# Kernel tuning notes

Measured on AMD Instinct MI355X. Metric: run time of the kernel, lower is better.

## Reference

```python
import jax, jax.numpy as jnp
import numpy as np

B, N, E, H = 2, 4096, 512, 8
D = E // H  # head size


def setup_inputs() -> dict:
    key = jax.random.key(0)
    ks = jax.random.split(key, 11)
    s = 1.0 / np.sqrt(E)
    inp = {
        'q': jax.random.normal(ks[0], (B, N, E), jnp.float32),
        'k': jax.random.normal(ks[1], (B, N, E), jnp.float32),
        'v': jax.random.normal(ks[2], (B, N, E), jnp.float32),
        'Wq': jax.random.uniform(ks[3], (E, E), jnp.float32, -s, s),
        'bq': jax.random.uniform(ks[4], (E,), jnp.float32, -s, s),
        'Wk': jax.random.uniform(ks[5], (E, E), jnp.float32, -s, s),
        'bk': jax.random.uniform(ks[6], (E,), jnp.float32, -s, s),
        'Wv': jax.random.uniform(ks[7], (E, E), jnp.float32, -s, s),
        'bv': jax.random.uniform(ks[8], (E,), jnp.float32, -s, s),
        'Wo': jax.random.uniform(ks[9], (E, E), jnp.float32, -s, s),
        'bo': jax.random.uniform(ks[10], (E,), jnp.float32, -s, s),
    }
    return inp


def reference(q, k, v, Wq, bq, Wk, bk, Wv, bv, Wo, bo):
    # Linear projections (torch Linear: x @ W.T + b)
    qp = (q @ Wq.T + bq).reshape(B, N, H, D).transpose(0, 2, 1, 3)  # [B,H,N,D]
    kp = (k @ Wk.T + bk).reshape(B, N, H, D).transpose(0, 2, 1, 3)
    vp = (v @ Wv.T + bv).reshape(B, N, H, D).transpose(0, 2, 1, 3)
    scores = jnp.einsum('bhnd,bhmd->bhnm', qp, kp) / jnp.sqrt(jnp.float32(D))
    attn = jax.nn.softmax(scores, axis=-1)
    out = jnp.einsum('bhnm,bhmd->bhnd', attn, vp)  # [B,H,N,D]
    out = out.transpose(0, 2, 1, 3).reshape(B, N, E)
    return out @ Wo.T + bo
```

## Files before the change

kernel.cpp:

```cpp
#include <hip/hip_runtime.h>
#include <hip/hip_bf16.h>
#include <cstddef>
#include <cstdint>


typedef __bf16 bf16_t;
typedef __bf16 bf16x8 __attribute__((ext_vector_type(8)));
typedef __bf16 bf16x4 __attribute__((ext_vector_type(4)));
typedef float  f32x4  __attribute__((ext_vector_type(4)));

#define MFMA_BF16 __builtin_amdgcn_mfma_f32_16x16x32_bf16

static __device__ __forceinline__ bf16x8 cvt2(const float4& a, const float4& b) {
  return bf16x8{(bf16_t)a.x,(bf16_t)a.y,(bf16_t)a.z,(bf16_t)a.w,
                (bf16_t)b.x,(bf16_t)b.y,(bf16_t)b.z,(bf16_t)b.w};
}

static __device__ __forceinline__ uint32_t pk2(float a, float b) {
  uint32_t r;
  asm("v_cvt_pk_bf16_f32 %0, %1, %2" : "=v"(r) : "v"(a), "v"(b));
  return r;
}

__global__ void __launch_bounds__(256)
cvt_bf16(const float* __restrict__ q, const float* __restrict__ k,
         const float* __restrict__ v, const float* __restrict__ Wq,
         const float* __restrict__ Wk, const float* __restrict__ Wv,
         const float* __restrict__ Wo,
         bf16_t* __restrict__ qb, bf16_t* __restrict__ kb,
         bf16_t* __restrict__ vb, bf16_t* __restrict__ wq,
         bf16_t* __restrict__ wk, bf16_t* __restrict__ wv,
         bf16_t* __restrict__ wo)
{
  const int CQ = 524288;
  const int CW = 32768;
  const int TOT = 3 * CQ + 4 * CW;
  const int STRIDE = 2048 * 256;
  for (int c = blockIdx.x * 256 + threadIdx.x; c < TOT; c += STRIDE) {
    const float* src; bf16_t* dst; int off;
    if (c < 3 * CQ) {
      const int t = c >> 19;
      const int r = c & (CQ - 1);
      src = (t == 0) ? q : (t == 1) ? k : v;
      dst = (t == 0) ? qb : (t == 1) ? kb : vb;
      off = r << 3;
    } else {
      const int c2 = c - 3 * CQ;
      const int t = c2 >> 15;
      const int r = c2 & (CW - 1);
      src = (t == 0) ? Wq : (t == 1) ? Wk : (t == 2) ? Wv : Wo;
      dst = (t == 0) ? wq : (t == 1) ? wk : (t == 2) ? wv : wo;
      off = r << 3;
    }
    const float4 a = *(const float4*)(src + off);
    const float4 b = *(const float4*)(src + off + 4);
    *(bf16x8*)(dst + off) = cvt2(a, b);
  }
}

__global__ void __launch_bounds__(256, 3)
qkv_proj(const bf16_t* __restrict__ qb, const bf16_t* __restrict__ kb,
         const bf16_t* __restrict__ vb,
         const bf16_t* __restrict__ Wqb, const float* __restrict__ bq,
         const bf16_t* __restrict__ Wkb, const float* __restrict__ bk,
         const bf16_t* __restrict__ Wvb, const float* __restrict__ bv,
         bf16_t* __restrict__ Qp, bf16_t* __restrict__ Kp,
         bf16_t* __restrict__ Vt, float qscale)
{
  __shared__ __align__(16) bf16_t S[2 * 128 * 72];
  bf16_t* As = S;
  bf16_t* Bs = S + 128 * 72;

  const int l     = blockIdx.x;
  const int slice = l >> 8;
  const int inner = l & 255;
  const int mtile = ((inner >> 5) << 3) | (inner & 7);
  const int ntile = (inner >> 3) & 3;
  const int tid   = threadIdx.x;
  const int w     = tid >> 6;
  const int lane  = tid & 63;
  const int lr    = lane & 15;
  const int quad  = lane >> 4;
  const int wm    = w & 1;
  const int wn    = w >> 1;
  const int xrow  = tid >> 1, xcol = (tid & 1) << 5;

  const bf16_t* Xb   = (slice == 0) ? qb  : (slice == 1) ? kb  : vb;
  const bf16_t* W    = (slice == 0) ? Wqb : (slice == 1) ? Wkb : Wvb;
  const float*  bias = (slice == 0) ? bq  : (slice == 1) ? bk  : bv;
  const float scale  = (slice == 0) ? qscale : 1.0f;

  float bvv[4];
#pragma unroll
  for (int ci = 0; ci < 4; ++ci) bvv[ci] = bias[ntile * 128 + wn * 64 + ci * 16 + lr];

  f32x4 acc[4][4] = {};
  bf16x8 xa[4], wa[4];

#pragma unroll
  for (int j = 0; j < 4; ++j) {
    xa[j] = *(const bf16x8*)(Xb + (size_t)(mtile * 128 + xrow) * 512 + xcol + j * 8);
    wa[j] = *(const bf16x8*)(W  + (size_t)(ntile * 128 + xrow) * 512 + xcol + j * 8);
  }
#pragma unroll
  for (int j = 0; j < 4; ++j) {
    *(bf16x8*)(&As[xrow * 72 + xcol + j * 8]) = xa[j];
    *(bf16x8*)(&Bs[xrow * 72 + xcol + j * 8]) = wa[j];
  }
  __syncthreads();

  for (int it = 0; it < 8; ++it) {
    if (it != 7) {
      const int k0 = (it + 1) << 6;
#pragma unroll
      for (int j = 0; j < 4; ++j) {
        xa[j] = *(const bf16x8*)(Xb + (size_t)(mtile * 128 + xrow) * 512 + k0 + xcol + j * 8);
        wa[j] = *(const bf16x8*)(W  + (size_t)(ntile * 128 + xrow) * 512 + k0 + xcol + j * 8);
      }
    }
    bf16x8 af[4][2], bfr[4][2];
#pragma unroll
    for (int mi = 0; mi < 4; ++mi)
#pragma unroll
      for (int kh = 0; kh < 2; ++kh)
        af[mi][kh] = *(const bf16x8*)(&As[(wm * 64 + mi * 16 + lr) * 72 + (kh * 4 + quad) * 8]);
#pragma unroll
    for (int ci = 0; ci < 4; ++ci)
#pragma unroll
      for (int kh = 0; kh < 2; ++kh)
        bfr[ci][kh] = *(const bf16x8*)(&Bs[(wn * 64 + ci * 16 + lr) * 72 + (kh * 4 + quad) * 8]);
#pragma unroll
    for (int mi = 0; mi < 4; ++mi)
#pragma unroll
      for (int ci = 0; ci < 4; ++ci) {
        acc[mi][ci] = MFMA_BF16(af[mi][0], bfr[ci][0], acc[mi][ci], 0, 0, 0);
        acc[mi][ci] = MFMA_BF16(af[mi][1], bfr[ci][1], acc[mi][ci], 0, 0, 0);
      }
    __syncthreads();
    if (it != 7) {
#pragma unroll
      for (int j = 0; j < 4; ++j) {
        *(bf16x8*)(&As[xrow * 72 + xcol + j * 8]) = xa[j];
        *(bf16x8*)(&Bs[xrow * 72 + xcol + j * 8]) = wa[j];
      }
      __syncthreads();
    }
  }

  bf16_t (*Ct)[136] = (bf16_t (*)[136])S;
  if (slice < 2) {
    bf16_t* outQK = (slice == 0) ? Qp : Kp;
#pragma unroll
    for (int mi = 0; mi < 4; ++mi)
#pragma unroll
      for (int ci = 0; ci < 4; ++ci)
#pragma unroll
        for (int r = 0; r < 4; ++r)
          Ct[wm * 64 + mi * 16 + quad * 4 + r][wn * 64 + ci * 16 + lr] =
              (bf16_t)((acc[mi][ci][r] + bvv[ci]) * scale);
    __syncthreads();
    const int r2 = tid >> 1, half = tid & 1;
    const int gm = mtile * 128 + r2;
    const int b = gm >> 12, n = gm & 4095;
    const int gc0 = ntile * 128 + half * 64;
    const int h = gc0 >> 6;
    bf16_t* dst = outQK + (size_t)((b * 8 + h) * 4096 + n) * 64;
#pragma unroll
    for (int j = 0; j < 8; ++j)
      *(bf16x8*)(dst + j * 8) = *(const bf16x8*)(&Ct[r2][half * 64 + j * 8]);
  } else {
#pragma unroll
    for (int mi = 0; mi < 4; ++mi)
#pragma unroll
      for (int ci = 0; ci < 4; ++ci)
#pragma unroll
        for (int r = 0; r < 4; ++r)
          Ct[wn * 64 + ci * 16 + lr][wm * 64 + mi * 16 + quad * 4 + r] =
              (bf16_t)(acc[mi][ci][r] + bvv[ci]);
    __syncthreads();
    const int dline = tid >> 1, half = tid & 1;
    const int gc = ntile * 128 + dline;
    const int h = gc >> 6, dd = gc & 63;
    const int b = (mtile * 128) >> 12;
    const int n0 = (mtile * 128) & 4095;
    bf16_t* dst = Vt + (size_t)((b * 8 + h) * 64 + dd) * 4096 + n0 + half * 64;
#pragma unroll
    for (int j = 0; j < 8; ++j)
      *(bf16x8*)(dst + j * 8) = *(const bf16x8*)(&Ct[dline][half * 64 + j * 8]);
  }
}

__global__ void __launch_bounds__(256, 4)
o_proj(const bf16_t* __restrict__ Xb, const bf16_t* __restrict__ W,
       const float* __restrict__ bias, float* __restrict__ out)
{
  __shared__ __align__(16) bf16_t As[64 * 72];
  __shared__ __align__(16) bf16_t Bs[64 * 72];
  const int l     = blockIdx.x;
  const int mtile = l >> 3;
  const int ntile = l & 7;
  const int tid   = threadIdx.x;
  const int w     = tid >> 6;
  const int lane  = tid & 63;
  const int lr    = lane & 15;
  const int quad  = lane >> 4;
  const int wm    = w & 1;
  const int wn    = w >> 1;
  const int xrow  = tid >> 2, xcol = (tid & 3) << 4;

  float bvv[2];
#pragma unroll
  for (int ci = 0; ci < 2; ++ci) bvv[ci] = bias[ntile * 64 + wn * 32 + ci * 16 + lr];

  f32x4 acc[2][2] = {};
  bf16x8 xb[2], wb[2];

#pragma unroll
  for (int j = 0; j < 2; ++j) {
    xb[j] = *(const bf16x8*)(Xb + (size_t)(mtile * 64 + xrow) * 512 + xcol + j * 8);
    wb[j] = *(const bf16x8*)(W  + (size_t)(ntile * 64 + xrow) * 512 + xcol + j * 8);
  }
#pragma unroll
  for (int j = 0; j < 2; ++j) {
    *(bf16x8*)(&As[xrow * 72 + xcol + j * 8]) = xb[j];
    *(bf16x8*)(&Bs[xrow * 72 + xcol + j * 8]) = wb[j];
  }
  __syncthreads();

  for (int it = 0; it < 8; ++it) {
    if (it != 7) {
      const int k0 = (it + 1) << 6;
#pragma unroll
      for (int j = 0; j < 2; ++j) {
        xb[j] = *(const bf16x8*)(Xb + (size_t)(mtile * 64 + xrow) * 512 + k0 + xcol + j * 8);
        wb[j] = *(const bf16x8*)(W  + (size_t)(ntile * 64 + xrow) * 512 + k0 + xcol + j * 8);
      }
    }
    bf16x8 af[2][2], bfr[2][2];
#pragma unroll
    for (int mi = 0; mi < 2; ++mi)
#pragma unroll
      for (int kh = 0; kh < 2; ++kh)
        af[mi][kh] = *(const bf16x8*)(&As[(wm * 32 + mi * 16 + lr) * 72 + (kh * 4 + quad) * 8]);
#pragma unroll
    for (int ci = 0; ci < 2; ++ci)
#pragma unroll
      for (int kh = 0; kh < 2; ++kh)
        bfr[ci][kh] = *(const bf16x8*)(&Bs[(wn * 32 + ci * 16 + lr) * 72 + (kh * 4 + quad) * 8]);
#pragma unroll
    for (int mi = 0; mi < 2; ++mi)
#pragma unroll
      for (int ci = 0; ci < 2; ++ci) {
        acc[mi][ci] = MFMA_BF16(af[mi][0], bfr[ci][0], acc[mi][ci], 0, 0, 0);
        acc[mi][ci] = MFMA_BF16(af[mi][1], bfr[ci][1], acc[mi][ci], 0, 0, 0);
      }
    __syncthreads();
    if (it != 7) {
#pragma unroll
      for (int j = 0; j < 2; ++j) {
        *(bf16x8*)(&As[xrow * 72 + xcol + j * 8]) = xb[j];
        *(bf16x8*)(&Bs[xrow * 72 + xcol + j * 8]) = wb[j];
      }
      __syncthreads();
    }
  }

#pragma unroll
  for (int mi = 0; mi < 2; ++mi) {
    const int gm0 = mtile * 64 + wm * 32 + mi * 16 + quad * 4;
#pragma unroll
    for (int ci = 0; ci < 2; ++ci) {
      const int gc = ntile * 64 + wn * 32 + ci * 16 + lr;
#pragma unroll
      for (int r = 0; r < 4; ++r)
        out[(size_t)(gm0 + r) * 512 + gc] = acc[mi][ci][r] + bvv[ci];
    }
  }
}

__global__ void __launch_bounds__(128, 1)
flash_attn(const bf16_t* __restrict__ Qp, const bf16_t* __restrict__ Kp,
           const bf16_t* __restrict__ Vt, bf16_t* __restrict__ Oc)
{
  __shared__ __align__(16) bf16_t Klds[2][64 * 72];
  __shared__ __align__(16) bf16_t Vlds[2][64 * 72];

  const int tid  = threadIdx.x;
  const int w    = tid >> 6;
  const int lane = tid & 63, lr = lane & 15, quad = lane >> 4;
  const int bh   = blockIdx.x;
  const int qt0  = blockIdx.y * 128 + w * 64;

  const bf16_t* Qh = Qp + (size_t)bh * 4096 * 64;
  const bf16_t* Kh = Kp + (size_t)bh * 4096 * 64;
  const bf16_t* Vh = Vt + (size_t)bh * 64 * 4096;

  const int srow = tid >> 2;
  const int scol = (tid & 3) << 4;

  bf16x8 qf[4][2];
#pragma unroll
  for (int qi = 0; qi < 4; ++qi)
#pragma unroll
    for (int kh = 0; kh < 2; ++kh)
      qf[qi][kh] = *(const bf16x8*)(Qh + (size_t)(qt0 + qi * 16 + lr) * 64 + kh * 32 + quad * 8);

  bf16x8 kst[4], vst[4];
#pragma unroll
  for (int rr = 0; rr < 2; ++rr)
#pragma unroll
    for (int j = 0; j < 2; ++j) {
      kst[rr * 2 + j] = *(const bf16x8*)(Kh + (size_t)(srow + rr * 32) * 64 + scol + j * 8);
      vst[rr * 2 + j] = *(const bf16x8*)(Vh + (size_t)(srow + rr * 32) * 4096 + scol + j * 8);
    }
#pragma unroll
  for (int rr = 0; rr < 2; ++rr)
#pragma unroll
    for (int j = 0; j < 2; ++j) {
      *(bf16x8*)(&Klds[0][(srow + rr * 32) * 72 + scol + j * 8]) = kst[rr * 2 + j];
      *(bf16x8*)(&Vlds[0][(srow + rr * 32) * 72 + scol + j * 8]) = vst[rr * 2 + j];
    }
  __syncthreads();

  f32x4 acc[4][4] = {};
  float lsum[4] = {0.f, 0.f, 0.f, 0.f};
  const f32x4 zero = {0.f, 0.f, 0.f, 0.f};

  for (int it = 0; it < 64; ++it) {
    const int cur = it & 1, nxt = cur ^ 1;

    if (it != 63) {
      const int kvn = (it + 1) << 6;
#pragma unroll
      for (int rr = 0; rr < 2; ++rr)
#pragma unroll
        for (int j = 0; j < 2; ++j) {
          kst[rr * 2 + j] = *(const bf16x8*)(Kh + (size_t)(kvn + srow + rr * 32) * 64 + scol + j * 8);
          vst[rr * 2 + j] = *(const bf16x8*)(Vh + (size_t)(srow + rr * 32) * 4096 + kvn + scol + j * 8);
        }
    }

#pragma unroll
    for (int half = 0; half < 2; ++half) {
      bf16x8 kf[2][2];
#pragma unroll
      for (int mm = 0; mm < 2; ++mm)
#pragma unroll
        for (int kh = 0; kh < 2; ++kh)
          kf[mm][kh] = *(const bf16x8*)(&Klds[cur][((half * 2 + mm) * 16 + lr) * 72 + (kh * 4 + quad) * 8]);

      bf16x8 vf[4];
#pragma unroll
      for (int t = 0; t < 4; ++t)
        vf[t] = *(const bf16x8*)(&Vlds[cur][(t * 16 + lr) * 72 + (half * 4 + quad) * 8]);

      f32x4 sT[2][4];
#pragma unroll
      for (int mm = 0; mm < 2; ++mm)
#pragma unroll
        for (int qi = 0; qi < 4; ++qi) {
          sT[mm][qi] = MFMA_BF16(kf[mm][0], qf[qi][0], zero, 0, 0, 0);
          sT[mm][qi] = MFMA_BF16(kf[mm][1], qf[qi][1], sT[mm][qi], 0, 0, 0);
        }

      bf16x8 pa[4];
#pragma unroll
      for (int qi = 0; qi < 4; ++qi) {
        uint32_t a0, a1, b0, b1;
        {
          float p0 = __builtin_amdgcn_exp2f(sT[0][qi][0]);
          float p1 = __builtin_amdgcn_exp2f(sT[0][qi][1]);
          float p2 = __builtin_amdgcn_exp2f(sT[0][qi][2]);
          float p3 = __builtin_amdgcn_exp2f(sT[0][qi][3]);
          lsum[qi] += (p0 + p1) + (p2 + p3);
          a0 = pk2(p0, p1); b0 = pk2(p2, p3);
        }
        {
          float p0 = __builtin_amdgcn_exp2f(sT[1][qi][0]);
          float p1 = __builtin_amdgcn_exp2f(sT[1][qi][1]);
          float p2 = __builtin_amdgcn_exp2f(sT[1][qi][2]);
          float p3 = __builtin_amdgcn_exp2f(sT[1][qi][3]);
          lsum[qi] += (p0 + p1) + (p2 + p3);
          a1 = pk2(p0, p1); b1 = pk2(p2, p3);
        }
        uint32_t xa_ = a0, ya_ = a1;
        asm("v_permlane32_swap_b32 %0, %1" : "+v"(xa_), "+v"(ya_));
        asm("v_permlane16_swap_b32 %0, %1" : "+v"(xa_), "+v"(ya_));
        uint32_t xb_ = b0, yb_ = b1;
        asm("v_permlane32_swap_b32 %0, %1" : "+v"(xb_), "+v"(yb_));
        asm("v_permlane16_swap_b32 %0, %1" : "+v"(xb_), "+v"(yb_));
        union { uint32_t u[4]; bf16x8 v; } pu;
        pu.u[0] = xa_; pu.u[1] = xb_; pu.u[2] = ya_; pu.u[3] = yb_;
        pa[qi] = pu.v;
      }

#pragma unroll
      for (int t = 0; t < 4; ++t)
#pragma unroll
        for (int qi = 0; qi < 4; ++qi)
          acc[qi][t] = MFMA_BF16(pa[qi], vf[t], acc[qi][t], 0, 0, 0);
    }

    if (it != 63) {
#pragma unroll
      for (int rr = 0; rr < 2; ++rr)
#pragma unroll
        for (int j = 0; j < 2; ++j) {
          *(bf16x8*)(&Klds[nxt][(srow + rr * 32) * 72 + scol + j * 8]) = kst[rr * 2 + j];
          *(bf16x8*)(&Vlds[nxt][(srow + rr * 32) * 72 + scol + j * 8]) = vst[rr * 2 + j];
        }
    }
    __syncthreads();
  }

#pragma unroll
  for (int qi = 0; qi < 4; ++qi) {
    lsum[qi] += __shfl_xor(lsum[qi], 16);
    lsum[qi] += __shfl_xor(lsum[qi], 32);
  }

  const int b = bh >> 3, h = bh & 7;
  bf16_t* Ob = Oc + (size_t)b * 4096 * 512 + h * 64;
#pragma unroll
  for (int qi = 0; qi < 4; ++qi) {
    float inv[4];
#pragma unroll
    for (int r = 0; r < 4; ++r)
      inv[r] = 1.0f / __shfl(lsum[qi], quad * 4 + r);
#pragma unroll
    for (int t = 0; t < 4; ++t)
#pragma unroll
      for (int r = 0; r < 4; ++r) {
        const int n = qt0 + qi * 16 + quad * 4 + r;
        Ob[(size_t)n * 512 + t * 16 + lr] = (bf16_t)(acc[qi][t][r] * inv[r]);
      }
  }
}

extern "C" void kernel_launch(void* const* d_in, const int* in_sizes, int n_in,
                              void* d_out, int out_size, void* d_ws, size_t ws_size,
                              hipStream_t stream)
{
  const float* q  = (const float*)d_in[0];
  const float* k  = (const float*)d_in[1];
  const float* v  = (const float*)d_in[2];
  const float* Wq = (const float*)d_in[3];
  const float* bq = (const float*)d_in[4];
  const float* Wk = (const float*)d_in[5];
  const float* bk = (const float*)d_in[6];
  const float* Wv = (const float*)d_in[7];
  const float* bv = (const float*)d_in[8];
  const float* Wo = (const float*)d_in[9];
  const float* bo = (const float*)d_in[10];

  const size_t HEAD_ELEMS = (size_t)2 * 8 * 4096 * 64;
  const size_t W_ELEMS    = (size_t)512 * 512;

  bf16_t* base = (bf16_t*)d_ws;
  bf16_t* qb  = base;
  bf16_t* kb  = qb + HEAD_ELEMS;
  bf16_t* vb  = kb + HEAD_ELEMS;
  bf16_t* Qp  = vb + HEAD_ELEMS;
  bf16_t* Kp  = Qp + HEAD_ELEMS;
  bf16_t* Vt  = Kp + HEAD_ELEMS;
  bf16_t* wqb = Vt + HEAD_ELEMS;
  bf16_t* wkb = wqb + W_ELEMS;
  bf16_t* wvb = wkb + W_ELEMS;
  bf16_t* wob = wvb + W_ELEMS;
  bf16_t* Oc  = qb;

  const float qscale = 0.125f * 1.44269504f;

  cvt_bf16<<<dim3(2048), 256, 0, stream>>>(q, k, v, Wq, Wk, Wv, Wo,
                                           qb, kb, vb, wqb, wkb, wvb, wob);
  qkv_proj<<<dim3(768), 256, 0, stream>>>(qb, kb, vb, wqb, bq, wkb, bk,
                                          wvb, bv, Qp, Kp, Vt, qscale);
  flash_attn<<<dim3(16, 32), 128, 0, stream>>>(Qp, Kp, Vt, Oc);
  o_proj<<<dim3(1024), 256, 0, stream>>>(Oc, wob, bo, (float*)d_out);
}
```

Before: 246.2 us.

## Widen flash-attn blocks to four waves, coalesce projection stores, remap tile order

Flash attention now runs 256-thread blocks covering 256 query rows, so each K/V tile loaded into LDS is shared by four waves instead of two, and each thread stages half as much data. The QK projection epilogue is rearranged so that adjacent lanes write contiguous 16-byte chunks. The o_proj output is staged through an LDS float tile and written as float4 rows. The block-to-tile mapping in both GEMMs is also permuted to change cache locality. The cost is more LDS and registers per block, fewer blocks for flash attention, and a different L2 reuse pattern.

```diff
diff --git a/kernel.cpp b/kernel.cpp
--- a/kernel.cpp
+++ b/kernel.cpp
@@ -74,7 +74,7 @@
   const int l     = blockIdx.x;
   const int slice = l >> 8;
   const int inner = l & 255;
-  const int mtile = ((inner >> 5) << 3) | (inner & 7);
+  const int mtile = ((inner & 7) << 3) | (inner >> 5);
   const int ntile = (inner >> 3) & 3;
   const int tid   = threadIdx.x;
   const int w     = tid >> 6;
@@ -159,15 +159,17 @@
           Ct[wm * 64 + mi * 16 + quad * 4 + r][wn * 64 + ci * 16 + lr] =
               (bf16_t)((acc[mi][ci][r] + bvv[ci]) * scale);
     __syncthreads();
-    const int r2 = tid >> 1, half = tid & 1;
-    const int gm = mtile * 128 + r2;
-    const int b = gm >> 12, n = gm & 4095;
-    const int gc0 = ntile * 128 + half * 64;
-    const int h = gc0 >> 6;
-    bf16_t* dst = outQK + (size_t)((b * 8 + h) * 4096 + n) * 64;
-#pragma unroll
-    for (int j = 0; j < 8; ++j)
-      *(bf16x8*)(dst + j * 8) = *(const bf16x8*)(&Ct[r2][half * 64 + j * 8]);
+    const int j8 = lane >> 3, slot = lane & 7;
+#pragma unroll
+    for (int p = 0; p < 8; ++p) {
+      const int R = p * 32 + w * 8 + j8;
+      const int row = R >> 1, colHalf = R & 1;
+      const int gm = mtile * 128 + row;
+      const int b = gm >> 12, n = gm & 4095;
+      const int h = ntile * 2 + colHalf;
+      *(bf16x8*)(outQK + (size_t)((b * 8 + h) * 4096 + n) * 64 + slot * 8) =
+          *(const bf16x8*)(&Ct[row][colHalf * 64 + slot * 8]);
+    }
   } else {
 #pragma unroll
     for (int mi = 0; mi < 4; ++mi)
@@ -196,9 +198,10 @@
 {
   __shared__ __align__(16) bf16_t As[64 * 72];
   __shared__ __align__(16) bf16_t Bs[64 * 72];
+  __shared__ __align__(16) float  Cf[64 * 68];
   const int l     = blockIdx.x;
-  const int mtile = l >> 3;
-  const int ntile = l & 7;
+  const int mtile = ((l & 7) << 4) | ((l >> 3) & 15);
+  const int ntile = l >> 7;
   const int tid   = threadIdx.x;
   const int w     = tid >> 6;
   const int lane  = tid & 63;
@@ -266,19 +269,24 @@
   }
 
 #pragma unroll
-  for (int mi = 0; mi < 2; ++mi) {
-    const int gm0 = mtile * 64 + wm * 32 + mi * 16 + quad * 4;
-#pragma unroll
-    for (int ci = 0; ci < 2; ++ci) {
-      const int gc = ntile * 64 + wn * 32 + ci * 16 + lr;
+  for (int mi = 0; mi < 2; ++mi)
+#pragma unroll
+    for (int ci = 0; ci < 2; ++ci)
 #pragma unroll
       for (int r = 0; r < 4; ++r)
-        out[(size_t)(gm0 + r) * 512 + gc] = acc[mi][ci][r] + bvv[ci];
-    }
-  }
-}
-
-__global__ void __launch_bounds__(128, 1)
+        Cf[(wm * 32 + mi * 16 + quad * 4 + r) * 68 + (wn * 32 + ci * 16 + lr)] =
+            acc[mi][ci][r] + bvv[ci];
+  __syncthreads();
+#pragma unroll
+  for (int p = 0; p < 4; ++p) {
+    const int idx = p * 256 + tid;
+    const int row = idx >> 4, c4 = idx & 15;
+    const float4 v = *(const float4*)(&Cf[row * 68 + c4 * 4]);
+    *(float4*)(out + (size_t)(mtile * 64 + row) * 512 + ntile * 64 + c4 * 4) = v;
+  }
+}
+
+__global__ void __launch_bounds__(256, 3)
 flash_attn(const bf16_t* __restrict__ Qp, const bf16_t* __restrict__ Kp,
            const bf16_t* __restrict__ Vt, bf16_t* __restrict__ Oc)
 {
@@ -289,7 +297,7 @@
   const int w    = tid >> 6;
   const int lane = tid & 63, lr = lane & 15, quad = lane >> 4;
   const int bh   = blockIdx.x;
-  const int qt0  = blockIdx.y * 128 + w * 64;
+  const int qt0  = blockIdx.y * 256 + w * 64;
 
   const bf16_t* Qh = Qp + (size_t)bh * 4096 * 64;
   const bf16_t* Kh = Kp + (size_t)bh * 4096 * 64;
@@ -305,21 +313,17 @@
     for (int kh = 0; kh < 2; ++kh)
       qf[qi][kh] = *(const bf16x8*)(Qh + (size_t)(qt0 + qi * 16 + lr) * 64 + kh * 32 + quad * 8);
 
-  bf16x8 kst[4], vst[4];
-#pragma unroll
-  for (int rr = 0; rr < 2; ++rr)
-#pragma unroll
-    for (int j = 0; j < 2; ++j) {
-      kst[rr * 2 + j] = *(const bf16x8*)(Kh + (size_t)(srow + rr * 32) * 64 + scol + j * 8);
-      vst[rr * 2 + j] = *(const bf16x8*)(Vh + (size_t)(srow + rr * 32) * 4096 + scol + j * 8);
-    }
-#pragma unroll
-  for (int rr = 0; rr < 2; ++rr)
-#pragma unroll
-    for (int j = 0; j < 2; ++j) {
-      *(bf16x8*)(&Klds[0][(srow + rr * 32) * 72 + scol + j * 8]) = kst[rr * 2 + j];
-      *(bf16x8*)(&Vlds[0][(srow + rr * 32) * 72 + scol + j * 8]) = vst[rr * 2 + j];
-    }
+  bf16x8 kst[2], vst[2];
+#pragma unroll
+  for (int j = 0; j < 2; ++j) {
+    kst[j] = *(const bf16x8*)(Kh + (size_t)srow * 64 + scol + j * 8);
+    vst[j] = *(const bf16x8*)(Vh + (size_t)srow * 4096 + scol + j * 8);
+  }
+#pragma unroll
+  for (int j = 0; j < 2; ++j) {
+    *(bf16x8*)(&Klds[0][srow * 72 + scol + j * 8]) = kst[j];
+    *(bf16x8*)(&Vlds[0][srow * 72 + scol + j * 8]) = vst[j];
+  }
   __syncthreads();
 
   f32x4 acc[4][4] = {};
@@ -332,12 +336,10 @@
     if (it != 63) {
       const int kvn = (it + 1) << 6;
 #pragma unroll
-      for (int rr = 0; rr < 2; ++rr)
-#pragma unroll
-        for (int j = 0; j < 2; ++j) {
-          kst[rr * 2 + j] = *(const bf16x8*)(Kh + (size_t)(kvn + srow + rr * 32) * 64 + scol + j * 8);
-          vst[rr * 2 + j] = *(const bf16x8*)(Vh + (size_t)(srow + rr * 32) * 4096 + kvn + scol + j * 8);
-        }
+      for (int j = 0; j < 2; ++j) {
+        kst[j] = *(const bf16x8*)(Kh + (size_t)(kvn + srow) * 64 + scol + j * 8);
+        vst[j] = *(const bf16x8*)(Vh + (size_t)srow * 4096 + kvn + scol + j * 8);
+      }
     }
 
 #pragma unroll
@@ -403,12 +405,10 @@
 
     if (it != 63) {
 #pragma unroll
-      for (int rr = 0; rr < 2; ++rr)
-#pragma unroll
-        for (int j = 0; j < 2; ++j) {
-          *(bf16x8*)(&Klds[nxt][(srow + rr * 32) * 72 + scol + j * 8]) = kst[rr * 2 + j];
-          *(bf16x8*)(&Vlds[nxt][(srow + rr * 32) * 72 + scol + j * 8]) = vst[rr * 2 + j];
-        }
+      for (int j = 0; j < 2; ++j) {
+        *(bf16x8*)(&Klds[nxt][srow * 72 + scol + j * 8]) = kst[j];
+        *(bf16x8*)(&Vlds[nxt][srow * 72 + scol + j * 8]) = vst[j];
+      }
     }
     __syncthreads();
   }
@@ -475,6 +475,6 @@
                                            qb, kb, vb, wqb, wkb, wvb, wob);
   qkv_proj<<<dim3(768), 256, 0, stream>>>(qb, kb, vb, wqb, bq, wkb, bk,
                                           wvb, bv, Qp, Kp, Vt, qscale);
-  flash_attn<<<dim3(16, 32), 128, 0, stream>>>(Qp, Kp, Vt, Oc);
+  flash_attn<<<dim3(16, 16), 256, 0, stream>>>(Qp, Kp, Vt, Oc);
   o_proj<<<dim3(1024), 256, 0, stream>>>(Oc, wob, bo, (float*)d_out);
 }
```

Measured after the change: 394.0 us. 1.6x slower.
